# Kernel tuning notes

Hardware: AMD Instinct MI355X
Metric: run time of the kernel (lower is better)

Reference implementation:

```python
import jax, jax.numpy as jnp
import numpy as np

EMBED_DIM = 768
NUM_HEADS = 12
HEAD_DIM = EMBED_DIM // NUM_HEADS
D_FF = 4 * EMBED_DIM
EPS = 1e-6


def setup_inputs() -> dict:
    key = jax.random.key(0)
    ks = jax.random.split(key, 16)
    B, N, D = 4, 1024, EMBED_DIM
    s = 0.02
    return {
        "x": jax.random.normal(ks[0], (B, N, D), jnp.float32),
        "ln1_g": jnp.ones((D,), jnp.float32),
        "ln1_b": jnp.zeros((D,), jnp.float32),
        "Wq": jax.random.normal(ks[1], (D, D), jnp.float32) * s,
        "bq": jnp.zeros((D,), jnp.float32),
        "Wk": jax.random.normal(ks[2], (D, D), jnp.float32) * s,
        "bk": jnp.zeros((D,), jnp.float32),
        "Wv": jax.random.normal(ks[3], (D, D), jnp.float32) * s,
        "bv": jnp.zeros((D,), jnp.float32),
        "Wo": jax.random.normal(ks[4], (D, D), jnp.float32) * s,
        "bo": jnp.zeros((D,), jnp.float32),
        "ln2_g": jnp.ones((D,), jnp.float32),
        "ln2_b": jnp.zeros((D,), jnp.float32),
        "W1": jax.random.normal(ks[5], (D, D_FF), jnp.float32) * s,
        "b1": jnp.zeros((D_FF,), jnp.float32),
        "W2": jax.random.normal(ks[6], (D_FF, D), jnp.float32) * s,
        "b2": jnp.zeros((D,), jnp.float32),
    }


def _layernorm(x, g, b):
    mu = jnp.mean(x, axis=-1, keepdims=True)
    var = jnp.mean(jnp.square(x - mu), axis=-1, keepdims=True)
    return (x - mu) * jax.lax.rsqrt(var + EPS) * g + b


def _block(x, ln1_g, ln1_b, Wq, bq, Wk, bk, Wv, bv, Wo, bo,
           ln2_g, ln2_b, W1, b1, W2, b2):
    B, N, D = x.shape
    h = x
    xn = _layernorm(x, ln1_g, ln1_b)
    # [B, H, N, d]
    q = (xn @ Wq + bq).reshape(B, N, NUM_HEADS, HEAD_DIM).transpose(0, 2, 1, 3)
    k = (xn @ Wk + bk).reshape(B, N, NUM_HEADS, HEAD_DIM).transpose(0, 2, 1, 3)
    v = (xn @ Wv + bv).reshape(B, N, NUM_HEADS, HEAD_DIM).transpose(0, 2, 1, 3)
    scores = jnp.einsum('bhqd,bhkd->bhqk', q, k) / np.sqrt(HEAD_DIM).astype(x.dtype)
    probs = jax.nn.softmax(scores, axis=-1)
    ctx = jnp.einsum('bhqk,bhkd->bhqd', probs, v)
    ctx = ctx.transpose(0, 2, 1, 3).reshape(B, N, D)
    attn_out = ctx @ Wo + bo
    x = attn_out + h
    h = x
    xn = _layernorm(x, ln2_g, ln2_b)
    mlp = jax.nn.gelu(xn @ W1 + b1, approximate=False) @ W2 + b2
    return mlp + h


def reference(x, ln1_g, ln1_b, Wq, bq, Wk, bk, Wv, bv, Wo, bo,
              ln2_g, ln2_b, W1, b1, W2, b2):
    return _block(x, ln1_g, ln1_b, Wq, bq, Wk, bk, Wv, bv, Wo, bo,
                  ln2_g, ln2_b, W1, b1, W2, b2)
```

## Files before the change

kernel.cpp:

```cpp
#include <hip/hip_runtime.h>

typedef __bf16 bf16_t;
typedef bf16_t bf16x8 __attribute__((ext_vector_type(8)));
typedef float f32x4 __attribute__((ext_vector_type(4)));
typedef unsigned short us8 __attribute__((ext_vector_type(8)));

#define DEV static __device__ __forceinline__

DEV unsigned short f2bf(float f) {
  unsigned int x = __float_as_uint(f);
  return (unsigned short)((x + 0x7fffu + ((x >> 16) & 1u)) >> 16);
}

DEV f32x4 mfma16(bf16x8 a, bf16x8 b, f32x4 c) {
  return __builtin_amdgcn_mfma_f32_16x16x32_bf16(a, b, c, 0, 0, 0);
}

DEV void gload_lds16(const void* g, void* l) {
  __builtin_amdgcn_global_load_lds(
      (const __attribute__((address_space(1))) void*)g,
      (__attribute__((address_space(3))) void*)l, 16, 0, 0);
}

__global__ __launch_bounds__(256) void wt_transpose(
    const float* __restrict__ src, unsigned short* __restrict__ dst, int K, int N) {
  __shared__ float tile[32][33];
  int bx = blockIdx.x * 32;
  int by = blockIdx.y * 32;
  int tx = threadIdx.x, ty = threadIdx.y;
#pragma unroll
  for (int i = ty; i < 32; i += 8)
    tile[i][tx] = src[(size_t)(by + i) * N + bx + tx];
  __syncthreads();
#pragma unroll
  for (int i = ty; i < 32; i += 8)
    dst[(size_t)(bx + i) * K + by + tx] = f2bf(tile[tx][i]);
}

__global__ __launch_bounds__(256) void ln_kernel(
    const float* __restrict__ x, const float* __restrict__ gw,
    const float* __restrict__ bw, unsigned short* __restrict__ out) {
  int row = blockIdx.x;
  const float* xr = x + (size_t)row * 768;
  int t = threadIdx.x;
  float v0 = xr[t], v1 = xr[t + 256], v2 = xr[t + 512];
  float s = v0 + v1 + v2, sq = v0 * v0 + v1 * v1 + v2 * v2;
#pragma unroll
  for (int m = 1; m < 64; m <<= 1) { s += __shfl_xor(s, m); sq += __shfl_xor(sq, m); }
  __shared__ float ssum[4], ssq[4];
  int wid = t >> 6;
  if ((t & 63) == 0) { ssum[wid] = s; ssq[wid] = sq; }
  __syncthreads();
  s = ssum[0] + ssum[1] + ssum[2] + ssum[3];
  sq = ssq[0] + ssq[1] + ssq[2] + ssq[3];
  float mu = s * (1.f / 768.f);
  float var = sq * (1.f / 768.f) - mu * mu;
  float rstd = rsqrtf(fmaxf(var, 0.f) + 1e-6f);
  unsigned short* orow = out + (size_t)row * 768;
  orow[t]       = f2bf((v0 - mu) * rstd * gw[t]       + bw[t]);
  orow[t + 256] = f2bf((v1 - mu) * rstd * gw[t + 256] + bw[t + 256]);
  orow[t + 512] = f2bf((v2 - mu) * rstd * gw[t + 512] + bw[t + 512]);
}

template <int EPI>
__global__ __launch_bounds__(256) void gemm_bt(
    const unsigned short* __restrict__ A, const unsigned short* __restrict__ Bt, int K,
    const float* __restrict__ b0p, const float* __restrict__ b1p, const float* __restrict__ b2p,
    void* __restrict__ o0, void* __restrict__ o1, void* __restrict__ o2) {
  __shared__ unsigned short lA[128 * 32];
  __shared__ unsigned short lB[128 * 32];
  int tid = threadIdx.x;
  int wid = tid >> 6, lane = tid & 63;
  int bm = blockIdx.y * 128, bn = blockIdx.x * 128;
  int wr = (wid >> 1) * 64, wc = (wid & 1) * 64;

  f32x4 acc[4][4] = {};

  const unsigned short* ga  = A  + (size_t)(bm + (tid >> 2)) * K + (tid & 3) * 8;
  const unsigned short* ga2 = A  + (size_t)(bm + 64 + (tid >> 2)) * K + (tid & 3) * 8;
  const unsigned short* gb  = Bt + (size_t)(bn + (tid >> 2)) * K + (tid & 3) * 8;
  const unsigned short* gb2 = Bt + (size_t)(bn + 64 + (tid >> 2)) * K + (tid & 3) * 8;

  for (int kt = 0; kt < K; kt += 32) {
    __syncthreads();
    gload_lds16(ga,  (char*)lA + wid * 1024);
    gload_lds16(ga2, (char*)lA + 4096 + wid * 1024);
    gload_lds16(gb,  (char*)lB + wid * 1024);
    gload_lds16(gb2, (char*)lB + 4096 + wid * 1024);
    ga += 32; ga2 += 32; gb += 32; gb2 += 32;
    __syncthreads();
    bf16x8 af[4], bfv[4];
#pragma unroll
    for (int mi = 0; mi < 4; mi++)
      af[mi] = *(const bf16x8*)(lA + (wr + mi * 16 + (lane & 15)) * 32 + (lane >> 4) * 8);
#pragma unroll
    for (int ni = 0; ni < 4; ni++)
      bfv[ni] = *(const bf16x8*)(lB + (wc + ni * 16 + (lane & 15)) * 32 + (lane >> 4) * 8);
#pragma unroll
    for (int mi = 0; mi < 4; mi++)
#pragma unroll
      for (int ni = 0; ni < 4; ni++)
        acc[mi][ni] = mfma16(af[mi], bfv[ni], acc[mi][ni]);
  }

  int r0 = bm + wr + ((lane >> 4) << 2);
  int c0 = bn + wc + (lane & 15);
#pragma unroll
  for (int mi = 0; mi < 4; mi++) {
#pragma unroll
    for (int ni = 0; ni < 4; ni++) {
      int col = c0 + ni * 16;
#pragma unroll
      for (int r = 0; r < 4; r++) {
        int row = r0 + mi * 16 + r;
        float val = acc[mi][ni][r];
        if constexpr (EPI == 0) {
          int which = col / 768;
          int rem = col - which * 768;
          int h = rem >> 6, d = rem & 63;
          const float* bias = (which == 0) ? b0p : (which == 1) ? b1p : b2p;
          unsigned short* dst = (unsigned short*)((which == 0) ? o0 : (which == 1) ? o1 : o2);
          val += bias[rem];
          if (which == 0) val *= 0.125f;
          int b = row >> 10, n = row & 1023;
          dst[(((size_t)b * 12 + h) * 1024 + n) * 64 + d] = f2bf(val);
        } else {
          float hv = val + b0p[col];
          float ge = 0.5f * hv * (1.f + erff(hv * 0.70710678118654752f));
          ((unsigned short*)o0)[(size_t)row * 3072 + col] = f2bf(ge);
        }
      }
    }
  }
}

__global__ __launch_bounds__(256) void gemm_sk(
    const unsigned short* __restrict__ A, const unsigned short* __restrict__ Bt,
    int K, int ksplit, float* __restrict__ part) {
  __shared__ unsigned short lA[128 * 32];
  __shared__ unsigned short lB[64 * 32];
  int tid = threadIdx.x;
  int wid = tid >> 6, lane = tid & 63;
  int bm = blockIdx.y * 128, bn = blockIdx.x * 64;
  int k0 = blockIdx.z * ksplit;
  int wr = (wid >> 1) * 64, wc = (wid & 1) * 32;

  f32x4 acc[4][2] = {};

  const unsigned short* ga  = A  + (size_t)(bm + (tid >> 2)) * K + k0 + (tid & 3) * 8;
  const unsigned short* ga2 = A  + (size_t)(bm + 64 + (tid >> 2)) * K + k0 + (tid & 3) * 8;
  const unsigned short* gb  = Bt + (size_t)(bn + (tid >> 2)) * K + k0 + (tid & 3) * 8;

  for (int kt = 0; kt < ksplit; kt += 32) {
    __syncthreads();
    gload_lds16(ga,  (char*)lA + wid * 1024);
    gload_lds16(ga2, (char*)lA + 4096 + wid * 1024);
    gload_lds16(gb,  (char*)lB + wid * 1024);
    ga += 32; ga2 += 32; gb += 32;
    __syncthreads();
    bf16x8 af[4], bfv[2];
#pragma unroll
    for (int mi = 0; mi < 4; mi++)
      af[mi] = *(const bf16x8*)(lA + (wr + mi * 16 + (lane & 15)) * 32 + (lane >> 4) * 8);
#pragma unroll
    for (int ni = 0; ni < 2; ni++)
      bfv[ni] = *(const bf16x8*)(lB + (wc + ni * 16 + (lane & 15)) * 32 + (lane >> 4) * 8);
#pragma unroll
    for (int mi = 0; mi < 4; mi++)
#pragma unroll
      for (int ni = 0; ni < 2; ni++)
        acc[mi][ni] = mfma16(af[mi], bfv[ni], acc[mi][ni]);
  }

  float* pp = part + (size_t)blockIdx.z * (4096 * 768);
  int r0 = bm + wr + ((lane >> 4) << 2);
  int c0 = bn + wc + (lane & 15);
#pragma unroll
  for (int mi = 0; mi < 4; mi++)
#pragma unroll
    for (int ni = 0; ni < 2; ni++)
#pragma unroll
      for (int r = 0; r < 4; r++)
        pp[(size_t)(r0 + mi * 16 + r) * 768 + c0 + ni * 16] = acc[mi][ni][r];
}

__global__ __launch_bounds__(256) void skred(
    const float* __restrict__ part, const float* __restrict__ bias,
    const float* __restrict__ resid, float* __restrict__ out) {
  int i = blockIdx.x * 256 + threadIdx.x;
  const f32x4* p0 = (const f32x4*)part;
  const f32x4* p1 = p0 + 786432;
  const f32x4* rz = (const f32x4*)resid;
  const f32x4* bz = (const f32x4*)bias;
  f32x4 v = p0[i] + p1[i] + bz[i % 192] + rz[i];
  ((f32x4*)out)[i] = v;
}

__global__ __launch_bounds__(256) void attn_kernel(
    const unsigned short* __restrict__ q, const unsigned short* __restrict__ k,
    const unsigned short* __restrict__ v, unsigned short* __restrict__ ctx) {
  int bh = blockIdx.y;
  int bb = bh / 12, hh = bh % 12;
  int q0 = blockIdx.x * 64;
  int wid = threadIdx.x >> 6, lane = threadIdx.x & 63;
  const size_t head_off = (size_t)bh * 1024 * 64;
  const unsigned short* qh = q + head_off;
  const unsigned short* kh = k + head_off;
  const unsigned short* vh = v + head_off;

  __shared__ unsigned short lK[64 * 64];
  __shared__ unsigned short lVt[64][72];
  __shared__ unsigned short lP[4][16][72];

  bf16x8 aq[2];
  {
    int row = q0 + wid * 16 + (lane & 15);
    const unsigned short* qr = qh + (size_t)row * 64 + (lane >> 4) * 8;
    aq[0] = *(const bf16x8*)qr;
    aq[1] = *(const bf16x8*)(qr + 32);
  }
  f32x4 cacc[4] = {};
  float mrow[4], lrow[4];
#pragma unroll
  for (int r = 0; r < 4; r++) { mrow[r] = -1e30f; lrow[r] = 0.f; }

  for (int kt = 0; kt < 16; ++kt) {
    __syncthreads();
    {
      int t = threadIdx.x;
      int row = t >> 3;
      int colb = (t & 7) * 16;
      const unsigned short* g0 = kh + (size_t)(kt * 64 + row) * 64 + ((colb ^ ((row & 7) << 4)) >> 1);
      gload_lds16(g0, (char*)lK + wid * 1024);
      int row2 = row + 32;
      const unsigned short* g1 = kh + (size_t)(kt * 64 + row2) * 64 + ((colb ^ ((row & 7) << 4)) >> 1);
      gload_lds16(g1, (char*)lK + 4096 + wid * 1024);
    }
    {
      int kp = threadIdx.x >> 3;
      int d0 = (threadIdx.x & 7) * 8;
      const unsigned short* vp = vh + (size_t)(kt * 64 + kp * 2) * 64 + d0;
      us8 r0v = *(const us8*)vp;
      us8 r1v = *(const us8*)(vp + 64);
      unsigned int* lv = (unsigned int*)lVt;
#pragma unroll
      for (int j = 0; j < 8; j++)
        lv[(d0 + j) * 36 + kp] = (unsigned int)r0v[j] | ((unsigned int)r1v[j] << 16);
    }
    __syncthreads();

    f32x4 sacc[4] = {};
#pragma unroll
    for (int ni = 0; ni < 4; ni++) {
      int krow = ni * 16 + (lane & 15);
      int swz = (krow & 7) << 4;
      const char* base = (const char*)lK + krow * 128;
      bf16x8 b0 = *(const bf16x8*)(base + (((lane >> 4) * 16) ^ swz));
      bf16x8 b1 = *(const bf16x8*)(base + ((64 + (lane >> 4) * 16) ^ swz));
      sacc[ni] = mfma16(aq[0], b0, sacc[ni]);
      sacc[ni] = mfma16(aq[1], b1, sacc[ni]);
    }

    float pv[4][4];
#pragma unroll
    for (int r = 0; r < 4; r++) {
      float tm = fmaxf(fmaxf(sacc[0][r], sacc[1][r]), fmaxf(sacc[2][r], sacc[3][r]));
#pragma unroll
      for (int m = 1; m < 16; m <<= 1) tm = fmaxf(tm, __shfl_xor(tm, m));
      float mn = fmaxf(mrow[r], tm);
      float corr = __expf(mrow[r] - mn);
      float rs = 0.f;
#pragma unroll
      for (int ni = 0; ni < 4; ni++) {
        float p = __expf(sacc[ni][r] - mn);
        pv[ni][r] = p;
        rs += p;
      }
#pragma unroll
      for (int m = 1; m < 16; m <<= 1) rs += __shfl_xor(rs, m);
      lrow[r] = lrow[r] * corr + rs;
      mrow[r] = mn;
#pragma unroll
      for (int di = 0; di < 4; di++) cacc[di][r] *= corr;
    }

#pragma unroll
    for (int ni = 0; ni < 4; ni++)
#pragma unroll
      for (int r = 0; r < 4; r++)
        lP[wid][(lane >> 4) * 4 + r][ni * 16 + (lane & 15)] = f2bf(pv[ni][r]);

#pragma unroll
    for (int kc = 0; kc < 2; kc++) {
      bf16x8 pa = *(const bf16x8*)&lP[wid][lane & 15][kc * 32 + (lane >> 4) * 8];
#pragma unroll
      for (int di = 0; di < 4; di++) {
        bf16x8 bvv = *(const bf16x8*)&lVt[di * 16 + (lane & 15)][kc * 32 + (lane >> 4) * 8];
        cacc[di] = mfma16(pa, bvv, cacc[di]);
      }
    }
  }

#pragma unroll
  for (int di = 0; di < 4; di++)
#pragma unroll
    for (int r = 0; r < 4; r++)
      lP[wid][(lane >> 4) * 4 + r][di * 16 + (lane & 15)] = f2bf(cacc[di][r] / lrow[r]);
  {
    int row = lane >> 2;
    int c0 = (lane & 3) * 16;
    const unsigned short* sp = &lP[wid][row][c0];
    us8 w0 = *(const us8*)sp;
    us8 w1 = *(const us8*)(sp + 8);
    int gq = q0 + wid * 16 + row;
    unsigned short* gp = ctx + ((size_t)(bb * 1024 + gq)) * 768 + hh * 64 + c0;
    *(us8*)gp = w0;
    *(us8*)(gp + 8) = w1;
  }
}

extern "C" void kernel_launch(void* const* d_in, const int* in_sizes, int n_in,
                              void* d_out, int out_size, void* d_ws, size_t ws_size,
                              hipStream_t stream) {
  const float* x    = (const float*)d_in[0];
  const float* ln1g = (const float*)d_in[1];
  const float* ln1b = (const float*)d_in[2];
  const float* Wq   = (const float*)d_in[3];
  const float* bq   = (const float*)d_in[4];
  const float* Wk   = (const float*)d_in[5];
  const float* bk   = (const float*)d_in[6];
  const float* Wv   = (const float*)d_in[7];
  const float* bv   = (const float*)d_in[8];
  const float* Wo   = (const float*)d_in[9];
  const float* bo   = (const float*)d_in[10];
  const float* ln2g = (const float*)d_in[11];
  const float* ln2b = (const float*)d_in[12];
  const float* W1   = (const float*)d_in[13];
  const float* b1   = (const float*)d_in[14];
  const float* W2   = (const float*)d_in[15];
  const float* b2   = (const float*)d_in[16];
  float* out = (float*)d_out;

  char* ws = (char*)d_ws;
  unsigned short* xn    = (unsigned short*)(ws + 0);
  unsigned short* qws   = (unsigned short*)(ws + 6291456);
  unsigned short* kws   = (unsigned short*)(ws + 12582912);
  unsigned short* vws   = (unsigned short*)(ws + 18874368);
  float*          part  = (float*)(ws + 0);
  unsigned short* ctx   = (unsigned short*)(ws + 25165824);
  float*          x2    = (float*)(ws + 31457280);
  unsigned short* x2n   = (unsigned short*)(ws + 44040192);
  unsigned short* hmid  = (unsigned short*)(ws + 50331648);
  unsigned short* Wqkvt = (unsigned short*)(ws + 75497472);
  unsigned short* Wot   = (unsigned short*)(ws + 79036416);
  unsigned short* W1t   = (unsigned short*)(ws + 80216064);
  unsigned short* W2t   = (unsigned short*)(ws + 84934656);

  dim3 tb(32, 8);
  wt_transpose<<<dim3(24, 24), tb, 0, stream>>>(Wq, Wqkvt, 768, 768);
  wt_transpose<<<dim3(24, 24), tb, 0, stream>>>(Wk, Wqkvt + 589824, 768, 768);
  wt_transpose<<<dim3(24, 24), tb, 0, stream>>>(Wv, Wqkvt + 1179648, 768, 768);
  wt_transpose<<<dim3(24, 24), tb, 0, stream>>>(Wo, Wot, 768, 768);
  wt_transpose<<<dim3(96, 24), tb, 0, stream>>>(W1, W1t, 768, 3072);
  wt_transpose<<<dim3(24, 96), tb, 0, stream>>>(W2, W2t, 3072, 768);

  ln_kernel<<<4096, 256, 0, stream>>>(x, ln1g, ln1b, xn);
  gemm_bt<0><<<dim3(18, 32), 256, 0, stream>>>(xn, Wqkvt, 768, bq, bk, bv, qws, kws, vws);
  attn_kernel<<<dim3(16, 48), 256, 0, stream>>>(qws, kws, vws, ctx);
  gemm_sk<<<dim3(12, 32, 2), 256, 0, stream>>>(ctx, Wot, 768, 384, part);
  skred<<<3072, 256, 0, stream>>>(part, bo, x, x2);
  ln_kernel<<<4096, 256, 0, stream>>>(x2, ln2g, ln2b, x2n);
  gemm_bt<2><<<dim3(24, 32), 256, 0, stream>>>(x2n, W1t, 768, b1, nullptr, nullptr, hmid, nullptr, nullptr);
  gemm_sk<<<dim3(12, 32, 2), 256, 0, stream>>>(hmid, W2t, 3072, 1536, part);
  skred<<<3072, 256, 0, stream>>>(part, b2, x2, out);
}
```

Baseline: 336.8 us.

## Split attention KV range across two wave groups and merge softmax states

```diff
diff --git a/kernel.cpp b/kernel.cpp
--- a/kernel.cpp
+++ b/kernel.cpp
@@ -196,25 +196,29 @@
   ((f32x4*)out)[i] = v;
 }
 
-__global__ __launch_bounds__(256) void attn_kernel(
+__global__ __launch_bounds__(512) void attn_kernel(
     const unsigned short* __restrict__ q, const unsigned short* __restrict__ k,
     const unsigned short* __restrict__ v, unsigned short* __restrict__ ctx) {
+  __shared__ __align__(16) char smem[51200];
   int bh = blockIdx.y;
   int bb = bh / 12, hh = bh % 12;
   int q0 = blockIdx.x * 64;
-  int wid = threadIdx.x >> 6, lane = threadIdx.x & 63;
+  int tid = threadIdx.x;
+  int wid = tid >> 6, lane = tid & 63;
+  int grp = wid >> 2, wq = wid & 3;
+  int tg = tid & 255;
   const size_t head_off = (size_t)bh * 1024 * 64;
   const unsigned short* qh = q + head_off;
-  const unsigned short* kh = k + head_off;
-  const unsigned short* vh = v + head_off;
-
-  __shared__ unsigned short lK[64 * 64];
-  __shared__ unsigned short lVt[64][72];
-  __shared__ unsigned short lP[4][16][72];
+  const unsigned short* kh = k + head_off + (size_t)grp * 512 * 64;
+  const unsigned short* vh = v + head_off + (size_t)grp * 512 * 64;
+
+  unsigned short* lK  = (unsigned short*)smem + grp * 4096;
+  unsigned short* lVt = (unsigned short*)(smem + 16384) + grp * 4096;
+  unsigned short* lPw = (unsigned short*)(smem + 32768) + wid * 1152;
 
   bf16x8 aq[2];
   {
-    int row = q0 + wid * 16 + (lane & 15);
+    int row = q0 + wq * 16 + (lane & 15);
     const unsigned short* qr = qh + (size_t)row * 64 + (lane >> 4) * 8;
     aq[0] = *(const bf16x8*)qr;
     aq[1] = *(const bf16x8*)(qr + 32);
@@ -224,28 +228,30 @@
 #pragma unroll
   for (int r = 0; r < 4; r++) { mrow[r] = -1e30f; lrow[r] = 0.f; }
 
-  for (int kt = 0; kt < 16; ++kt) {
+  for (int kt = 0; kt < 8; ++kt) {
     __syncthreads();
     {
-      int t = threadIdx.x;
-      int row = t >> 3;
-      int colb = (t & 7) * 16;
-      const unsigned short* g0 = kh + (size_t)(kt * 64 + row) * 64 + ((colb ^ ((row & 7) << 4)) >> 1);
-      gload_lds16(g0, (char*)lK + wid * 1024);
-      int row2 = row + 32;
-      const unsigned short* g1 = kh + (size_t)(kt * 64 + row2) * 64 + ((colb ^ ((row & 7) << 4)) >> 1);
-      gload_lds16(g1, (char*)lK + 4096 + wid * 1024);
+      int row = tg >> 3;
+      int colb = (tg & 7) * 16;
+      int sw = (colb ^ ((row & 7) << 4)) >> 1;
+      const unsigned short* g0 = kh + (size_t)(kt * 64 + row) * 64 + sw;
+      gload_lds16(g0, (char*)lK + wq * 1024);
+      const unsigned short* g1 = kh + (size_t)(kt * 64 + row + 32) * 64 + sw;
+      gload_lds16(g1, (char*)lK + 4096 + wq * 1024);
     }
     {
-      int kp = threadIdx.x >> 3;
-      int d0 = (threadIdx.x & 7) * 8;
+      int kp = tg >> 3;
+      int d0 = (tg & 7) * 8;
       const unsigned short* vp = vh + (size_t)(kt * 64 + kp * 2) * 64 + d0;
       us8 r0v = *(const us8*)vp;
       us8 r1v = *(const us8*)(vp + 64);
       unsigned int* lv = (unsigned int*)lVt;
 #pragma unroll
-      for (int j = 0; j < 8; j++)
-        lv[(d0 + j) * 36 + kp] = (unsigned int)r0v[j] | ((unsigned int)r1v[j] << 16);
+      for (int j = 0; j < 8; j++) {
+        int d = d0 + j;
+        lv[d * 32 + (kp ^ ((((d >> 3) & 7)) << 2))] =
+            (unsigned int)r0v[j] | ((unsigned int)r1v[j] << 16);
+      }
     }
     __syncthreads();
 
@@ -288,31 +294,55 @@
     for (int ni = 0; ni < 4; ni++)
 #pragma unroll
       for (int r = 0; r < 4; r++)
-        lP[wid][(lane >> 4) * 4 + r][ni * 16 + (lane & 15)] = f2bf(pv[ni][r]);
+        lPw[((lane >> 4) * 4 + r) * 72 + ni * 16 + (lane & 15)] = f2bf(pv[ni][r]);
 
 #pragma unroll
     for (int kc = 0; kc < 2; kc++) {
-      bf16x8 pa = *(const bf16x8*)&lP[wid][lane & 15][kc * 32 + (lane >> 4) * 8];
+      bf16x8 pa = *(const bf16x8*)(lPw + (lane & 15) * 72 + kc * 32 + (lane >> 4) * 8);
 #pragma unroll
       for (int di = 0; di < 4; di++) {
-        bf16x8 bvv = *(const bf16x8*)&lVt[di * 16 + (lane & 15)][kc * 32 + (lane >> 4) * 8];
+        int row = di * 16 + (lane & 15);
+        int colu = (kc * 32 + (lane >> 4) * 8) ^ ((((row >> 3) & 7)) << 3);
+        bf16x8 bvv = *(const bf16x8*)(lVt + row * 64 + colu);
         cacc[di] = mfma16(pa, bvv, cacc[di]);
       }
     }
   }
 
-#pragma unroll
-  for (int di = 0; di < 4; di++)
-#pragma unroll
-    for (int r = 0; r < 4; r++)
-      lP[wid][(lane >> 4) * 4 + r][di * 16 + (lane & 15)] = f2bf(cacc[di][r] / lrow[r]);
-  {
+  __syncthreads();
+  float* mb = (float*)smem;
+  float* p = mb + (wq * 64 + lane) * 25;
+  if (grp == 1) {
+#pragma unroll
+    for (int di = 0; di < 4; di++)
+#pragma unroll
+      for (int r = 0; r < 4; r++) p[di * 4 + r] = cacc[di][r];
+#pragma unroll
+    for (int r = 0; r < 4; r++) { p[16 + r] = mrow[r]; p[20 + r] = lrow[r]; }
+  }
+  __syncthreads();
+  if (grp == 0) {
+#pragma unroll
+    for (int r = 0; r < 4; r++) {
+      float m1 = p[16 + r], l1 = p[20 + r];
+      float M = fmaxf(mrow[r], m1);
+      float a0 = __expf(mrow[r] - M), a1 = __expf(m1 - M);
+      lrow[r] = a0 * lrow[r] + a1 * l1;
+#pragma unroll
+      for (int di = 0; di < 4; di++)
+        cacc[di][r] = a0 * cacc[di][r] + a1 * p[di * 4 + r];
+    }
+#pragma unroll
+    for (int di = 0; di < 4; di++)
+#pragma unroll
+      for (int r = 0; r < 4; r++)
+        lPw[((lane >> 4) * 4 + r) * 72 + di * 16 + (lane & 15)] = f2bf(cacc[di][r] / lrow[r]);
     int row = lane >> 2;
     int c0 = (lane & 3) * 16;
-    const unsigned short* sp = &lP[wid][row][c0];
+    const unsigned short* sp = lPw + row * 72 + c0;
     us8 w0 = *(const us8*)sp;
     us8 w1 = *(const us8*)(sp + 8);
-    int gq = q0 + wid * 16 + row;
+    int gq = q0 + wq * 16 + row;
     unsigned short* gp = ctx + ((size_t)(bb * 1024 + gq)) * 768 + hh * 64 + c0;
     *(us8*)gp = w0;
     *(us8*)(gp + 8) = w1;
@@ -366,7 +396,7 @@
 
   ln_kernel<<<4096, 256, 0, stream>>>(x, ln1g, ln1b, xn);
   gemm_bt<0><<<dim3(18, 32), 256, 0, stream>>>(xn, Wqkvt, 768, bq, bk, bv, qws, kws, vws);
-  attn_kernel<<<dim3(16, 48), 256, 0, stream>>>(qws, kws, vws, ctx);
+  attn_kernel<<<dim3(16, 48), 512, 0, stream>>>(qws, kws, vws, ctx);
   gemm_sk<<<dim3(12, 32, 2), 256, 0, stream>>>(ctx, Wot, 768, 384, part);
   skred<<<3072, 256, 0, stream>>>(part, bo, x, x2);
   ln_kernel<<<4096, 256, 0, stream>>>(x2, ln2g, ln2b, x2n);
```

After: 331.7 us. No clear change (-1.5%).

## Widen attention blocks to 8 waves sharing K/V tiles and swizzle V^T LDS layout

Applied to the files above, without the earlier changes.

```diff
diff --git a/kernel.cpp b/kernel.cpp
--- a/kernel.cpp
+++ b/kernel.cpp
@@ -196,25 +196,27 @@
   ((f32x4*)out)[i] = v;
 }
 
-__global__ __launch_bounds__(256) void attn_kernel(
+__global__ __launch_bounds__(512) void attn_kernel(
     const unsigned short* __restrict__ q, const unsigned short* __restrict__ k,
     const unsigned short* __restrict__ v, unsigned short* __restrict__ ctx) {
+  __shared__ __align__(16) char smem[34816];
   int bh = blockIdx.y;
   int bb = bh / 12, hh = bh % 12;
-  int q0 = blockIdx.x * 64;
-  int wid = threadIdx.x >> 6, lane = threadIdx.x & 63;
+  int tid = threadIdx.x;
+  int wid = tid >> 6, lane = tid & 63;
+  int q0 = blockIdx.x * 128 + wid * 16;
   const size_t head_off = (size_t)bh * 1024 * 64;
   const unsigned short* qh = q + head_off;
   const unsigned short* kh = k + head_off;
   const unsigned short* vh = v + head_off;
 
-  __shared__ unsigned short lK[64 * 64];
-  __shared__ unsigned short lVt[64][72];
-  __shared__ unsigned short lP[4][16][72];
+  unsigned short* lK  = (unsigned short*)smem;
+  unsigned short* lVt = (unsigned short*)(smem + 8192);
+  unsigned short* lPw = (unsigned short*)(smem + 16384) + wid * 1152;
 
   bf16x8 aq[2];
   {
-    int row = q0 + wid * 16 + (lane & 15);
+    int row = q0 + (lane & 15);
     const unsigned short* qr = qh + (size_t)row * 64 + (lane >> 4) * 8;
     aq[0] = *(const bf16x8*)qr;
     aq[1] = *(const bf16x8*)(qr + 32);
@@ -224,28 +226,26 @@
 #pragma unroll
   for (int r = 0; r < 4; r++) { mrow[r] = -1e30f; lrow[r] = 0.f; }
 
+  int krow_s = tid >> 3;
+  int kcolb_s = (tid & 7) * 16;
+  int ksw = (kcolb_s ^ ((krow_s & 7) << 4)) >> 1;
+
   for (int kt = 0; kt < 16; ++kt) {
     __syncthreads();
-    {
-      int t = threadIdx.x;
-      int row = t >> 3;
-      int colb = (t & 7) * 16;
-      const unsigned short* g0 = kh + (size_t)(kt * 64 + row) * 64 + ((colb ^ ((row & 7) << 4)) >> 1);
-      gload_lds16(g0, (char*)lK + wid * 1024);
-      int row2 = row + 32;
-      const unsigned short* g1 = kh + (size_t)(kt * 64 + row2) * 64 + ((colb ^ ((row & 7) << 4)) >> 1);
-      gload_lds16(g1, (char*)lK + 4096 + wid * 1024);
-    }
-    {
-      int kp = threadIdx.x >> 3;
-      int d0 = (threadIdx.x & 7) * 8;
+    gload_lds16(kh + (size_t)(kt * 64 + krow_s) * 64 + ksw, (char*)lK + wid * 1024);
+    if (tid < 256) {
+      int kp = tid >> 3;
+      int d0 = (tid & 7) * 8;
       const unsigned short* vp = vh + (size_t)(kt * 64 + kp * 2) * 64 + d0;
       us8 r0v = *(const us8*)vp;
       us8 r1v = *(const us8*)(vp + 64);
       unsigned int* lv = (unsigned int*)lVt;
 #pragma unroll
-      for (int j = 0; j < 8; j++)
-        lv[(d0 + j) * 36 + kp] = (unsigned int)r0v[j] | ((unsigned int)r1v[j] << 16);
+      for (int j = 0; j < 8; j++) {
+        int d = d0 + j;
+        lv[d * 32 + (kp ^ ((((d >> 3) & 7)) << 2))] =
+            (unsigned int)r0v[j] | ((unsigned int)r1v[j] << 16);
+      }
     }
     __syncthreads();
 
@@ -288,14 +288,16 @@
     for (int ni = 0; ni < 4; ni++)
 #pragma unroll
       for (int r = 0; r < 4; r++)
-        lP[wid][(lane >> 4) * 4 + r][ni * 16 + (lane & 15)] = f2bf(pv[ni][r]);
+        lPw[((lane >> 4) * 4 + r) * 72 + ni * 16 + (lane & 15)] = f2bf(pv[ni][r]);
 
 #pragma unroll
     for (int kc = 0; kc < 2; kc++) {
-      bf16x8 pa = *(const bf16x8*)&lP[wid][lane & 15][kc * 32 + (lane >> 4) * 8];
+      bf16x8 pa = *(const bf16x8*)(lPw + (lane & 15) * 72 + kc * 32 + (lane >> 4) * 8);
 #pragma unroll
       for (int di = 0; di < 4; di++) {
-        bf16x8 bvv = *(const bf16x8*)&lVt[di * 16 + (lane & 15)][kc * 32 + (lane >> 4) * 8];
+        int row = di * 16 + (lane & 15);
+        int colu = (kc * 32 + (lane >> 4) * 8) ^ ((((row >> 3) & 7)) << 3);
+        bf16x8 bvv = *(const bf16x8*)(lVt + row * 64 + colu);
         cacc[di] = mfma16(pa, bvv, cacc[di]);
       }
     }
@@ -305,14 +307,14 @@
   for (int di = 0; di < 4; di++)
 #pragma unroll
     for (int r = 0; r < 4; r++)
-      lP[wid][(lane >> 4) * 4 + r][di * 16 + (lane & 15)] = f2bf(cacc[di][r] / lrow[r]);
+      lPw[((lane >> 4) * 4 + r) * 72 + di * 16 + (lane & 15)] = f2bf(cacc[di][r] / lrow[r]);
   {
     int row = lane >> 2;
     int c0 = (lane & 3) * 16;
-    const unsigned short* sp = &lP[wid][row][c0];
+    const unsigned short* sp = lPw + row * 72 + c0;
     us8 w0 = *(const us8*)sp;
     us8 w1 = *(const us8*)(sp + 8);
-    int gq = q0 + wid * 16 + row;
+    int gq = q0 + row;
     unsigned short* gp = ctx + ((size_t)(bb * 1024 + gq)) * 768 + hh * 64 + c0;
     *(us8*)gp = w0;
     *(us8*)(gp + 8) = w1;
@@ -366,7 +368,7 @@
 
   ln_kernel<<<4096, 256, 0, stream>>>(x, ln1g, ln1b, xn);
   gemm_bt<0><<<dim3(18, 32), 256, 0, stream>>>(xn, Wqkvt, 768, bq, bk, bv, qws, kws, vws);
-  attn_kernel<<<dim3(16, 48), 256, 0, stream>>>(qws, kws, vws, ctx);
+  attn_kernel<<<dim3(8, 48), 512, 0, stream>>>(qws, kws, vws, ctx);
   gemm_sk<<<dim3(12, 32, 2), 256, 0, stream>>>(ctx, Wot, 768, 384, part);
   skred<<<3072, 256, 0, stream>>>(part, bo, x, x2);
   ln_kernel<<<4096, 256, 0, stream>>>(x2, ln2g, ln2b, x2n);
```

Result: no change. 343.6 us (+2.0%).
